# Optimization experiments

Measured on AMD Instinct MI355X. Metric: run time of the kernel, lower is better.

Reference implementation:

```python
import jax, jax.numpy as jnp
import numpy as np

B = 1
L_IMG, L_TMP, L_TXT = 1024, 1024, 256
D, H, HD, MLP = 1024, 16, 64, 4096
L = L_TXT + L_IMG + L_TMP
EPS = 1e-6
ATTN_SCALE = float(1.0 / np.sqrt(HD))


def setup_inputs() -> dict:
    key = jax.random.key(0)
    ks = jax.random.split(key, 12)
    s = 0.02  # keep activations stable
    return {
        'img': jax.random.normal(ks[0], (B, L_IMG, D), jnp.float32),
        'temporal': jax.random.normal(ks[1], (B, L_TMP, D), jnp.float32),
        'txt': jax.random.normal(ks[2], (B, L_TXT, D), jnp.float32),
        'vec': jax.random.normal(ks[3], (B, D), jnp.float32),
        'pe': jax.random.normal(ks[4], (B, 1, L, HD // 2, 2, 2), jnp.float32),
        'mod_w': jax.random.normal(ks[5], (3, D, 6 * D), jnp.float32) * s,
        'mod_b': jnp.zeros((3, 6 * D), jnp.float32),
        'qkv_w': jax.random.normal(ks[6], (3, D, 3 * D), jnp.float32) * s,
        'q_scale': jnp.ones((3, HD), jnp.float32),
        'k_scale': jnp.ones((3, HD), jnp.float32),
        'proj_w': jax.random.normal(ks[7], (3, D, D), jnp.float32) * s,
        'proj_b': jnp.zeros((3, D), jnp.float32),
        'mlp_w1': jax.random.normal(ks[8], (3, D, MLP), jnp.float32) * s,
        'mlp_b1': jnp.zeros((3, MLP), jnp.float32),
        'mlp_w2': jax.random.normal(ks[9], (3, MLP, D), jnp.float32) * s,
        'mlp_b2': jnp.zeros((3, D), jnp.float32),
    }


def _ln(x):
    # LayerNorm, elementwise_affine=False, eps=1e-6
    m = jnp.mean(x, axis=-1, keepdims=True)
    v = jnp.mean((x - m) ** 2, axis=-1, keepdims=True)
    return (x - m) * jax.lax.rsqrt(v + EPS)


def _rms(x, scale):
    # flux QKNorm RMSNorm with learnable per-head-dim scale
    return x * jax.lax.rsqrt(jnp.mean(x * x, axis=-1, keepdims=True) + EPS) * scale


def _rope(x, pe):
    # x: (B,H,L,HD), pe: (B,1,L,HD//2,2,2)
    xr = x.reshape(*x.shape[:-1], -1, 1, 2)
    out = pe[..., 0] * xr[..., 0] + pe[..., 1] * xr[..., 1]  # (B,H,L,HD//2,2)
    return out.reshape(x.shape)


def _forward(img, temporal, txt, vec, pe, mod_w, mod_b, qkv_w, q_scale, k_scale,
             proj_w, proj_b, mlp_w1, mlp_b1, mlp_w2, mlp_b2):
    sv = jax.nn.silu(vec)  # (B,D)

    def mods(i):
        m = (sv @ mod_w[i] + mod_b[i])[:, None, :]  # (B,1,6D)
        return jnp.split(m, 6, axis=-1)  # shift1, scale1, gate1, shift2, scale2, gate2

    def qkv_stream(x, i, shift1, scale1):
        xm = (1.0 + scale1) * _ln(x) + shift1
        qkv = (xm @ qkv_w[i]).reshape(x.shape[0], x.shape[1], 3, H, HD)
        q, k, v = jnp.moveaxis(qkv, 2, 0)  # each (B,Ls,H,HD)
        q = jnp.swapaxes(q, 1, 2)
        k = jnp.swapaxes(k, 1, 2)
        v = jnp.swapaxes(v, 1, 2)  # (B,H,Ls,HD)
        return _rms(q, q_scale[i]), _rms(k, k_scale[i]), v

    i_sh1, i_sc1, i_g1, i_sh2, i_sc2, i_g2 = mods(0)
    t_sh1, t_sc1, t_g1, t_sh2, t_sc2, t_g2 = mods(1)
    x_sh1, x_sc1, x_g1, x_sh2, x_sc2, x_g2 = mods(2)

    img_q, img_k, img_v = qkv_stream(img, 0, i_sh1, i_sc1)
    tmp_q, tmp_k, tmp_v = qkv_stream(temporal, 1, t_sh1, t_sc1)
    txt_q, txt_k, txt_v = qkv_stream(txt, 2, x_sh1, x_sc1)

    q = jnp.concatenate((txt_q, img_q, tmp_q), axis=2)
    k = jnp.concatenate((txt_k, img_k, tmp_k), axis=2)
    # NOTE: faithful to source bug: v concat uses temporal_q, not temporal_v
    v = jnp.concatenate((txt_v, img_v, tmp_q), axis=2)

    q = _rope(q, pe)
    k = _rope(k, pe)
    scores = jnp.einsum('bhqd,bhkd->bhqk', q, k) * ATTN_SCALE
    attn = jnp.einsum('bhqk,bhkd->bhqd', jax.nn.softmax(scores, axis=-1), v)
    attn = jnp.swapaxes(attn, 1, 2).reshape(attn.shape[0], L, H * HD)  # (B,L,D)

    txt_a = attn[:, :L_TXT]
    img_a = attn[:, L_TXT:L_TXT + L_IMG]
    tmp_a = attn[:, L_TXT + L_IMG:]

    def mlp(x, i):
        return jax.nn.gelu(x @ mlp_w1[i] + mlp_b1[i], approximate=True) @ mlp_w2[i] + mlp_b2[i]

    img = img + i_g1 * (img_a @ proj_w[0] + proj_b[0])
    img = img + i_g2 * mlp((1.0 + i_sc2) * _ln(img) + i_sh2, 0)
    temporal = temporal + t_g1 * (tmp_a @ proj_w[1] + proj_b[1])
    # NOTE: faithful to source bug: temporal_norm2 is applied to (updated) img
    temporal = temporal + t_g2 * mlp((1.0 + t_sc2) * _ln(img) + t_sh2, 1)
    txt = txt + x_g1 * (txt_a @ proj_w[2] + proj_b[2])
    txt = txt + x_g2 * mlp((1.0 + x_sc2) * _ln(txt) + x_sh2, 2)
    return img, temporal, txt


def reference(img, temporal, txt, vec, pe, mod_w, mod_b, qkv_w, q_scale, k_scale,
              proj_w, proj_b, mlp_w1, mlp_b1, mlp_w2, mlp_b2):
    return _forward(img, temporal, txt, vec, pe, mod_w, mod_b, qkv_w, q_scale,
                    k_scale, proj_w, proj_b, mlp_w1, mlp_b1, mlp_w2, mlp_b2)
```

## Files before the change

### kernel.cpp

```cpp
#include <hip/hip_runtime.h>
#include <hip/hip_bf16.h>

#define L_TXT 256
#define L_IMG 1024
#define L_TMP 1024
#define LTOT  2304
#define DMODEL 1024
#define NH 16
#define HDIM 64
#define DMLP 4096
#define EPSV 1e-6f

typedef unsigned short ushort;
typedef __attribute__((ext_vector_type(8))) short short8b;
typedef __attribute__((ext_vector_type(8))) unsigned short ushort8v;
typedef __attribute__((ext_vector_type(4))) float f32x4;
typedef __attribute__((ext_vector_type(4))) unsigned short ushort4v;

#define MOD_OFF    ((size_t)0)
#define XM_OFF     ((size_t)73728)
#define QKV_OFF    ((size_t)4792320)
#define QB_OFF     ((size_t)18948096)
#define KB_OFF     ((size_t)23666688)
#define VTB_OFF    ((size_t)28385280)
#define ATT_OFF    ((size_t)33103872)
#define S1_OFF     ((size_t)37822464)
#define QKVWT_OFF  ((size_t)49356800)
#define PROJWT_OFF ((size_t)68231168)
#define W1T_OFF    ((size_t)74522624)
#define W2T_OFF    ((size_t)99688448)
#define W2T_END    ((size_t)124854272)

static __device__ __forceinline__ ushort f2bf(float x) {
    __hip_bfloat16 b = __float2bfloat16(x);
    return *reinterpret_cast<ushort*>(&b);
}
static __device__ __forceinline__ float bf2f(ushort u) {
    return __uint_as_float(((unsigned)u) << 16);
}

typedef __attribute__((address_space(1))) const unsigned char gas_t;
typedef __attribute__((address_space(3))) unsigned char las_t;
static __device__ __forceinline__ void gload16(const void* g, void* l) {
    __builtin_amdgcn_global_load_lds((gas_t*)g, (las_t*)l, 16, 0, 0);
}

__global__ __launch_bounds__(256) void k_conv(const float* __restrict__ vec,
                                              const float* __restrict__ modw,
                                              const float* __restrict__ modb,
                                              float* __restrict__ mod,
                                              const float* __restrict__ qkvw,
                                              const float* __restrict__ projw,
                                              const float* __restrict__ w1,
                                              const float* __restrict__ w2,
                                              ushort* __restrict__ qkvwt,
                                              ushort* __restrict__ projwt,
                                              ushort* __restrict__ w1t,
                                              ushort* __restrict__ w2t) {
    __shared__ float tb[64][65];
    int bid = blockIdx.x;
    int tid = threadIdx.x;
    if (bid < 144) {
        __shared__ float svs[DMODEL];
        __shared__ float pl[8][128];
        float4 vv = *reinterpret_cast<const float4*>(vec + tid*4);
        float4 sv4;
        sv4.x = vv.x / (1.0f + __expf(-vv.x));
        sv4.y = vv.y / (1.0f + __expf(-vv.y));
        sv4.z = vv.z / (1.0f + __expf(-vv.z));
        sv4.w = vv.w / (1.0f + __expf(-vv.w));
        *reinterpret_cast<float4*>(&svs[tid*4]) = sv4;
        __syncthreads();
        int g0 = bid * 128;
        int i  = g0 / 6144;
        int j0 = g0 - i * 6144;
        int jl = tid & 31, ko = tid >> 5;
        const float* wp = modw + (size_t)i * 1024 * 6144 + j0 + jl*4;
        float4 acc = {0.f,0.f,0.f,0.f};
        for (int kk = 0; kk < 128; kk++) {
            int k = kk*8 + ko;
            float4 wv = *reinterpret_cast<const float4*>(wp + (size_t)k * 6144);
            float s = svs[k];
            acc.x += s*wv.x; acc.y += s*wv.y; acc.z += s*wv.z; acc.w += s*wv.w;
        }
        pl[ko][jl*4+0] = acc.x; pl[ko][jl*4+1] = acc.y;
        pl[ko][jl*4+2] = acc.z; pl[ko][jl*4+3] = acc.w;
        __syncthreads();
        if (tid < 128) {
            float s = 0.f;
#pragma unroll
            for (int k = 0; k < 8; k++) s += pl[k][tid];
            mod[g0 + tid] = s + modb[g0 + tid];
        }
        return;
    }
    int b = bid - 144;
    const float* W; ushort* WT; int K, N, nt, kt;
    if (b < 2304) {
        int s = b / 768, r = b % 768;
        K = 1024; N = 3072; nt = r % 48; kt = r / 48;
        W = qkvw + (size_t)s * K * N; WT = qkvwt + (size_t)s * N * K;
    } else if (b < 3072) {
        b -= 2304; int s = b / 256, r = b % 256;
        K = 1024; N = 1024; nt = r % 16; kt = r / 16;
        W = projw + (size_t)s * K * N; WT = projwt + (size_t)s * N * K;
    } else if (b < 6144) {
        b -= 3072; int s = b / 1024, r = b % 1024;
        K = 1024; N = 4096; nt = r % 64; kt = r / 64;
        W = w1 + (size_t)s * K * N; WT = w1t + (size_t)s * N * K;
    } else {
        b -= 6144; int s = b / 1024, r = b % 1024;
        K = 4096; N = 1024; nt = r % 16; kt = r / 16;
        W = w2 + (size_t)s * K * N; WT = w2t + (size_t)s * N * K;
    }
    {
        int r = tid >> 4, c4 = (tid & 15) * 4;
#pragma unroll
        for (int i = 0; i < 4; i++) {
            float4 v = *reinterpret_cast<const float4*>(W + (size_t)(kt*64 + r + i*16) * N + nt*64 + c4);
            tb[r + i*16][c4+0] = v.x; tb[r + i*16][c4+1] = v.y;
            tb[r + i*16][c4+2] = v.z; tb[r + i*16][c4+3] = v.w;
        }
    }
    __syncthreads();
    {
        int n = tid >> 2, ks = (tid & 3) * 16;
        ushort8v u0, u1;
#pragma unroll
        for (int i = 0; i < 8; i++) u0[i] = f2bf(tb[ks+i][n]);
#pragma unroll
        for (int i = 0; i < 8; i++) u1[i] = f2bf(tb[ks+8+i][n]);
        ushort* dst = WT + (size_t)(nt*64 + n) * K + kt*64 + ks;
        *reinterpret_cast<ushort8v*>(dst)     = u0;
        *reinterpret_cast<ushort8v*>(dst + 8) = u1;
    }
}

__global__ __launch_bounds__(256) void k_conv_slice(const float* __restrict__ W,
                                                    ushort* __restrict__ WT,
                                                    int K, int N) {
    __shared__ float tb[64][65];
    int nt = blockIdx.x, kt = blockIdx.y, tid = threadIdx.x;
    {
        int r = tid >> 4, c4 = (tid & 15) * 4;
#pragma unroll
        for (int i = 0; i < 4; i++) {
            float4 v = *reinterpret_cast<const float4*>(W + (size_t)(kt*64 + r + i*16) * N + nt*64 + c4);
            tb[r + i*16][c4+0] = v.x; tb[r + i*16][c4+1] = v.y;
            tb[r + i*16][c4+2] = v.z; tb[r + i*16][c4+3] = v.w;
        }
    }
    __syncthreads();
    {
        int n = tid >> 2, ks = (tid & 3) * 16;
        ushort8v u0, u1;
#pragma unroll
        for (int i = 0; i < 8; i++) u0[i] = f2bf(tb[ks+i][n]);
#pragma unroll
        for (int i = 0; i < 8; i++) u1[i] = f2bf(tb[ks+8+i][n]);
        ushort* dst = WT + (size_t)(nt*64 + n) * K + kt*64 + ks;
        *reinterpret_cast<ushort8v*>(dst)     = u0;
        *reinterpret_cast<ushort8v*>(dst + 8) = u1;
    }
}

__global__ __launch_bounds__(256) void k_ln_mod1(const float* __restrict__ img,
                                                 const float* __restrict__ tmp,
                                                 const float* __restrict__ txt,
                                                 const float* __restrict__ mod,
                                                 ushort* __restrict__ xm) {
    int l = blockIdx.x;
    const float* src; int strm;
    if (l < L_TXT)              { src = txt + (size_t)l * DMODEL;            strm = 2; }
    else if (l < L_TXT + L_IMG) { src = img + (size_t)(l - L_TXT) * DMODEL;  strm = 0; }
    else                        { src = tmp + (size_t)(l - L_TXT - L_IMG) * DMODEL; strm = 1; }

    int d = threadIdx.x * 4;
    float4 x = *reinterpret_cast<const float4*>(src + d);
    float s  = x.x + x.y + x.z + x.w;
    float s2 = x.x*x.x + x.y*x.y + x.z*x.z + x.w*x.w;
#pragma unroll
    for (int o = 32; o > 0; o >>= 1) { s += __shfl_xor(s, o); s2 += __shfl_xor(s2, o); }
    __shared__ float red[8];
    int wave = threadIdx.x >> 6, lane = threadIdx.x & 63;
    if (lane == 0) { red[wave*2] = s; red[wave*2+1] = s2; }
    __syncthreads();
    if (threadIdx.x == 0) {
        float a = 0.f, b = 0.f;
        for (int w = 0; w < 4; w++) { a += red[w*2]; b += red[w*2+1]; }
        red[0] = a; red[1] = b;
    }
    __syncthreads();
    float mean = red[0] * (1.0f/DMODEL);
    float var  = red[1] * (1.0f/DMODEL) - mean*mean;
    float inv  = rsqrtf(var + EPSV);

    const float* sh = mod + strm*6144;
    const float* sc = sh + 1024;
    float4 shv = *reinterpret_cast<const float4*>(sh + d);
    float4 scv = *reinterpret_cast<const float4*>(sc + d);
    ushort4v o;
    o.x = f2bf((1.f+scv.x)*((x.x-mean)*inv) + shv.x);
    o.y = f2bf((1.f+scv.y)*((x.y-mean)*inv) + shv.y);
    o.z = f2bf((1.f+scv.z)*((x.z-mean)*inv) + shv.z);
    o.w = f2bf((1.f+scv.w)*((x.w-mean)*inv) + shv.w);
    *reinterpret_cast<ushort4v*>(xm + (size_t)l*DMODEL + d) = o;
}

__global__ __launch_bounds__(256) void k_ln_mod2(const float* __restrict__ src,
                                                 const float* __restrict__ sh,
                                                 const float* __restrict__ sc,
                                                 ushort* __restrict__ out) {
    int r = blockIdx.x;
    const float* srow = src + (size_t)r * DMODEL;
    int d = threadIdx.x * 4;
    float4 x = *reinterpret_cast<const float4*>(srow + d);
    float s  = x.x + x.y + x.z + x.w;
    float s2 = x.x*x.x + x.y*x.y + x.z*x.z + x.w*x.w;
#pragma unroll
    for (int o = 32; o > 0; o >>= 1) { s += __shfl_xor(s, o); s2 += __shfl_xor(s2, o); }
    __shared__ float red[8];
    int wave = threadIdx.x >> 6, lane = threadIdx.x & 63;
    if (lane == 0) { red[wave*2] = s; red[wave*2+1] = s2; }
    __syncthreads();
    if (threadIdx.x == 0) {
        float a = 0.f, b = 0.f;
        for (int w = 0; w < 4; w++) { a += red[w*2]; b += red[w*2+1]; }
        red[0] = a; red[1] = b;
    }
    __syncthreads();
    float mean = red[0] * (1.0f/DMODEL);
    float var  = red[1] * (1.0f/DMODEL) - mean*mean;
    float inv  = rsqrtf(var + EPSV);
    float4 shv = *reinterpret_cast<const float4*>(sh + d);
    float4 scv = *reinterpret_cast<const float4*>(sc + d);
    ushort4v o;
    o.x = f2bf((1.f+scv.x)*((x.x-mean)*inv) + shv.x);
    o.y = f2bf((1.f+scv.y)*((x.y-mean)*inv) + shv.y);
    o.z = f2bf((1.f+scv.z)*((x.z-mean)*inv) + shv.z);
    o.w = f2bf((1.f+scv.w)*((x.w-mean)*inv) + shv.w);
    *reinterpret_cast<ushort4v*>(out + (size_t)r*DMODEL + d) = o;
}

__global__ __launch_bounds__(256) void k_ln_modg(const float* __restrict__ s1,
                                                 const float* __restrict__ mod,
                                                 ushort* __restrict__ xm) {
    int row = blockIdx.x;
    int strm = row < 256 ? 2 : 0;
    const float* srow = s1 + (size_t)row * DMODEL;
    int d = threadIdx.x * 4;
    float4 x = *reinterpret_cast<const float4*>(srow + d);
    float s  = x.x + x.y + x.z + x.w;
    float s2 = x.x*x.x + x.y*x.y + x.z*x.z + x.w*x.w;
#pragma unroll
    for (int o = 32; o > 0; o >>= 1) { s += __shfl_xor(s, o); s2 += __shfl_xor(s2, o); }
    __shared__ float red[8];
    int wave = threadIdx.x >> 6, lane = threadIdx.x & 63;
    if (lane == 0) { red[wave*2] = s; red[wave*2+1] = s2; }
    __syncthreads();
    if (threadIdx.x == 0) {
        float a = 0.f, b = 0.f;
        for (int w = 0; w < 4; w++) { a += red[w*2]; b += red[w*2+1]; }
        red[0] = a; red[1] = b;
    }
    __syncthreads();
    float mean = red[0] * (1.0f/DMODEL);
    float var  = red[1] * (1.0f/DMODEL) - mean*mean;
    float inv  = rsqrtf(var + EPSV);
    const float* sh = mod + strm*6144 + 3*1024;
    const float* sc = mod + strm*6144 + 4*1024;
    float4 shv = *reinterpret_cast<const float4*>(sh + d);
    float4 scv = *reinterpret_cast<const float4*>(sc + d);
    ushort4v o;
    o.x = f2bf((1.f+scv.x)*((x.x-mean)*inv) + shv.x);
    o.y = f2bf((1.f+scv.y)*((x.y-mean)*inv) + shv.y);
    o.z = f2bf((1.f+scv.z)*((x.z-mean)*inv) + shv.z);
    o.w = f2bf((1.f+scv.w)*((x.w-mean)*inv) + shv.w);
    *reinterpret_cast<ushort4v*>(xm + (size_t)row*DMODEL + d) = o;
}

__device__ __forceinline__ float gelu_fast(float x) {
    return x / (1.0f + __expf(-1.5957691216057308f * (x + 0.044715f * x * x * x)));
}

template<int MODE, int BM, typename OutT>
__global__ __launch_bounds__(256) void k_gemm_ms(const ushort* __restrict__ A_t,
                                                 const ushort* __restrict__ A_i,
                                                 const ushort* __restrict__ A_m,
                                                 const ushort* __restrict__ BT,
                                                 const float* __restrict__ bias,
                                                 const float* __restrict__ res_t,
                                                 const float* __restrict__ res_i,
                                                 const float* __restrict__ res_m,
                                                 const float* __restrict__ mod, int gidx,
                                                 OutT* __restrict__ out_t,
                                                 OutT* __restrict__ out_i,
                                                 OutT* __restrict__ out_m,
                                                 int N, int K, int ry0) {
    constexpr int MI = BM / 32;
    const int brow = (ry0 + blockIdx.y) * BM;
    int s, lrow;
    if (brow < 256)       { s = 2; lrow = brow; }
    else if (brow < 1280) { s = 0; lrow = brow - 256; }
    else                  { s = 1; lrow = brow - 1280; }

    const ushort* A = (s==2 ? A_t : s==0 ? A_i : A_m) + (size_t)lrow * K;
    const ushort* BTs = BT + (size_t)s * N * K;
    const float* bi = bias ? bias + (size_t)s * N : nullptr;
    const float* resl = (MODE==2) ? ((s==2 ? res_t : s==0 ? res_i : res_m) + (size_t)lrow * N) : nullptr;
    const float* gate = (MODE==2) ? (mod + s*6144 + gidx*1024) : nullptr;
    OutT* Cl = (s==2 ? out_t : s==0 ? out_i : out_m) + (size_t)lrow * N;

    __shared__ ushort Asl[BM*64];
    __shared__ ushort Bsl[128*64];
    const int tid = threadIdx.x;
    const int lane = tid & 63, w = tid >> 6;
    const int wr = w >> 1, wc = w & 1;
    const int bn = blockIdx.x * 128;
    const int r15 = lane & 15, g4 = lane >> 4;

    f32x4 acc[MI][4];
#pragma unroll
    for (int i = 0; i < MI; i++)
#pragma unroll
        for (int j = 0; j < 4; j++) acc[i][j] = (f32x4){0.f,0.f,0.f,0.f};

    for (int k0 = 0; k0 < K; k0 += 64) {
#pragma unroll
        for (int i = 0; i < BM/32; i++) {
            int chunk = i*4 + w;
            int seg = chunk*64 + lane;
            int row = seg >> 3;
            int gs  = (seg & 7) ^ (row & 7);
            gload16(A + (size_t)row * K + k0 + gs*8, Asl + (size_t)chunk * 512);
        }
#pragma unroll
        for (int i = 0; i < 4; i++) {
            int chunk = i*4 + w;
            int seg = chunk*64 + lane;
            int row = seg >> 3;
            int gs  = (seg & 7) ^ (row & 7);
            gload16(BTs + (size_t)(bn + row) * K + k0 + gs*8, Bsl + (size_t)chunk * 512);
        }
        __syncthreads();
#pragma unroll
        for (int kk = 0; kk < 2; kk++) {
            short8b a[MI], b[4];
#pragma unroll
            for (int mi = 0; mi < MI; mi++) {
                int row = wr*(MI*16) + mi*16 + r15;
                int c   = kk*4 + g4;
                a[mi] = *reinterpret_cast<const short8b*>(&Asl[row*64 + ((c ^ (row & 7)))*8]);
            }
#pragma unroll
            for (int ni = 0; ni < 4; ni++) {
                int row = wc*64 + ni*16 + r15;
                int c   = kk*4 + g4;
                b[ni] = *reinterpret_cast<const short8b*>(&Bsl[row*64 + ((c ^ (row & 7)))*8]);
            }
#pragma unroll
            for (int mi = 0; mi < MI; mi++)
#pragma unroll
                for (int ni = 0; ni < 4; ni++)
                    acc[mi][ni] = __builtin_amdgcn_mfma_f32_16x16x32_bf16(a[mi], b[ni], acc[mi][ni], 0, 0, 0);
        }
        __syncthreads();
    }

#pragma unroll
    for (int mi = 0; mi < MI; mi++) {
#pragma unroll
        for (int ni = 0; ni < 4; ni++) {
            int col = bn + wc*64 + ni*16 + r15;
            float bv = bi ? bi[col] : 0.f;
#pragma unroll
            for (int r = 0; r < 4; r++) {
                int rr = wr*(MI*16) + mi*16 + g4*4 + r;
                float v = acc[mi][ni][r] + bv;
                if (MODE == 1) v = gelu_fast(v);
                if (MODE == 2) v = resl[(size_t)rr * N + col] + gate[col] * v;
                if (sizeof(OutT) == 2) Cl[(size_t)rr * N + col] = (OutT)f2bf(v);
                else                   Cl[(size_t)rr * N + col] = (OutT)v;
            }
        }
    }
}

__global__ __launch_bounds__(256) void k_qkvfin(const ushort* __restrict__ qkv,
                                                const float* __restrict__ pe,
                                                const float* __restrict__ qs,
                                                const float* __restrict__ ks,
                                                ushort* __restrict__ Q,
                                                ushort* __restrict__ K,
                                                ushort* __restrict__ VT) {
    const int tid = threadIdx.x;
    const int w = tid >> 6, lane = tid & 63;
    const int h  = blockIdx.x / 36;
    const int l0 = (blockIdx.x % 36) * 64;
    __shared__ ushort vbuf[64][65];

    for (int it = 0; it < 16; it++) {
        int ll = it*4 + w;
        int l = l0 + ll;
        int strm;
        if (l < L_TXT) strm = 2; else if (l < L_TXT + L_IMG) strm = 0; else strm = 1;
        const ushort* row = qkv + (size_t)l * 3 * DMODEL + h*HDIM + lane;
        float q = bf2f(row[0]);
        float k = bf2f(row[DMODEL]);
        float v = bf2f(row[2*DMODEL]);

        float sq = q*q, sk = k*k;
#pragma unroll
        for (int o = 32; o > 0; o >>= 1) { sq += __shfl_xor(sq, o); sk += __shfl_xor(sk, o); }
        float rq = q * rsqrtf(sq * (1.0f/HDIM) + EPSV) * qs[strm*HDIM + lane];
        float rk = k * rsqrtf(sk * (1.0f/HDIM) + EPSV) * ks[strm*HDIM + lane];

        float vout = (strm == 1) ? rq : v;

        float rq_p = __shfl_xor(rq, 1);
        float rk_p = __shfl_xor(rk, 1);
        float qe = (lane & 1) ? rq_p : rq;
        float qo = (lane & 1) ? rq : rq_p;
        float ke = (lane & 1) ? rk_p : rk;
        float ko = (lane & 1) ? rk : rk_p;
        const float* pel = pe + (size_t)l*128 + (lane >> 1)*4 + (lane & 1)*2;
        float qr = pel[0]*qe + pel[1]*qo;
        float kr = pel[0]*ke + pel[1]*ko;

        size_t idx = ((size_t)h * LTOT + l) * HDIM + lane;
        Q[idx] = f2bf(qr);
        K[idx] = f2bf(kr);
        vbuf[ll][lane] = f2bf(vout);
    }
    __syncthreads();
    {
        int d = tid >> 2, ls = (tid & 3) * 16;
        ushort8v u0, u1;
#pragma unroll
        for (int i = 0; i < 8; i++) u0[i] = vbuf[ls+i][d];
#pragma unroll
        for (int i = 0; i < 8; i++) u1[i] = vbuf[ls+8+i][d];
        ushort* dst = VT + ((size_t)h * 64 + d) * LTOT + l0 + ls;
        *reinterpret_cast<ushort8v*>(dst)     = u0;
        *reinterpret_cast<ushort8v*>(dst + 8) = u1;
    }
}

__global__ __launch_bounds__(256) void k_attn_mfma(const ushort* __restrict__ Qb,
                                                   const ushort* __restrict__ Kb,
                                                   const ushort* __restrict__ VTb,
                                                   ushort* __restrict__ att) {
    const int tid = threadIdx.x;
    const int w = tid >> 6, lane = tid & 63;
    const int h  = blockIdx.x / 36;
    const int qt = blockIdx.x % 36;
    const int qbase = qt*64 + w*16;
    const int g = lane >> 4;
    const int q = lane & 15;

    __shared__ ushort Ksl[2][64*64];
    __shared__ ushort Vsl[2][64*64];
    __shared__ ushort plds[4][1024];
    ushort* P = plds[w];

    const ushort* Kg = Kb  + (size_t)h * LTOT * 64;
    const ushort* Vg = VTb + (size_t)h * 64 * LTOT;

    const ushort* qp = Qb + ((size_t)h * LTOT + qbase + q) * 64 + g*8;
    const short8b qf0 = *reinterpret_cast<const short8b*>(qp);
    const short8b qf1 = *reinterpret_cast<const short8b*>(qp + 32);

    f32x4 out[4];
#pragma unroll
    for (int d = 0; d < 4; d++) out[d] = (f32x4){0.f,0.f,0.f,0.f};
    float m = -1e30f, lsum = 0.f;

#pragma unroll
    for (int i = 0; i < 2; i++) {
        int seg = i*256 + tid;
        int row = seg >> 3;
        int gs  = (seg & 7) ^ (row & 7);
        gload16(Kg + (size_t)row*64 + gs*8, &Ksl[0][(size_t)(i*256 + w*64)*8]);
        gload16(Vg + (size_t)row*LTOT + gs*8, &Vsl[0][(size_t)(i*256 + w*64)*8]);
    }

    for (int t = 0; t < 36; t++) {
        const int cb = t & 1;
        __syncthreads();
        if (t < 35) {
            int kvn = (t+1) * 64;
#pragma unroll
            for (int i = 0; i < 2; i++) {
                int seg = i*256 + tid;
                int row = seg >> 3;
                int gs  = (seg & 7) ^ (row & 7);
                gload16(Kg + (size_t)(kvn + row)*64 + gs*8, &Ksl[cb^1][(size_t)(i*256 + w*64)*8]);
                gload16(Vg + (size_t)row*LTOT + kvn + gs*8, &Vsl[cb^1][(size_t)(i*256 + w*64)*8]);
            }
        }

        f32x4 s[4];
        __builtin_amdgcn_s_setprio(1);
#pragma unroll
        for (int ks = 0; ks < 4; ks++) {
            int r = ks*16 + q;
            short8b kf0 = *reinterpret_cast<const short8b*>(&Ksl[cb][r*64 + ((g     ^ (r & 7)))*8]);
            short8b kf1 = *reinterpret_cast<const short8b*>(&Ksl[cb][r*64 + (((4+g) ^ (r & 7)))*8]);
            f32x4 acc = (f32x4){0.f,0.f,0.f,0.f};
            acc = __builtin_amdgcn_mfma_f32_16x16x32_bf16(kf0, qf0, acc, 0, 0, 0);
            acc = __builtin_amdgcn_mfma_f32_16x16x32_bf16(kf1, qf1, acc, 0, 0, 0);
            s[ks] = acc;
        }
        __builtin_amdgcn_s_setprio(0);
        float tmax = -1e30f;
#pragma unroll
        for (int ks = 0; ks < 4; ks++)
#pragma unroll
            for (int r = 0; r < 4; r++) tmax = fmaxf(tmax, s[ks][r]);
        tmax = fmaxf(tmax, __shfl_xor(tmax, 16));
        tmax = fmaxf(tmax, __shfl_xor(tmax, 32));
        float newm = fmaxf(m, tmax * 0.125f);
        float c = __expf(m - newm);
        float p[16];
        float tsum = 0.f;
#pragma unroll
        for (int ks = 0; ks < 4; ks++)
#pragma unroll
            for (int r = 0; r < 4; r++) {
                float pv = __expf(s[ks][r] * 0.125f - newm);
                p[ks*4+r] = pv;
                tsum += pv;
            }
        tsum += __shfl_xor(tsum, 16);
        tsum += __shfl_xor(tsum, 32);
        lsum = lsum * c + tsum;
        m = newm;
#pragma unroll
        for (int d = 0; d < 4; d++) out[d] *= c;

#pragma unroll
        for (int ks = 0; ks < 4; ks++) {
            ushort4v pk;
            pk.x = f2bf(p[ks*4+0]); pk.y = f2bf(p[ks*4+1]);
            pk.z = f2bf(p[ks*4+2]); pk.w = f2bf(p[ks*4+3]);
            int widx = (q*64 + ks*16 + g*4) ^ ((q & 7) << 3);
            *reinterpret_cast<ushort4v*>(&P[widx]) = pk;
        }
        __builtin_amdgcn_s_setprio(1);
#pragma unroll
        for (int c2 = 0; c2 < 2; c2++) {
            int ridx = (q*64 + c2*32 + g*8) ^ ((q & 7) << 3);
            short8b pf = *reinterpret_cast<const short8b*>(&P[ridx]);
#pragma unroll
            for (int ds = 0; ds < 4; ds++) {
                int d = ds*16 + q;
                short8b vf = *reinterpret_cast<const short8b*>(&Vsl[cb][d*64 + (((c2*4+g) ^ (d & 7)))*8]);
                out[ds] = __builtin_amdgcn_mfma_f32_16x16x32_bf16(vf, pf, out[ds], 0, 0, 0);
            }
        }
        __builtin_amdgcn_s_setprio(0);
    }

    float inv = 1.0f / lsum;
    ushort* orow = att + (size_t)(qbase + q) * DMODEL + h * HDIM;
#pragma unroll
    for (int ds = 0; ds < 4; ds++) {
        ushort4v o4;
        o4.x = f2bf(out[ds][0]*inv); o4.y = f2bf(out[ds][1]*inv);
        o4.z = f2bf(out[ds][2]*inv); o4.w = f2bf(out[ds][3]*inv);
        *reinterpret_cast<ushort4v*>(orow + ds*16 + g*4) = o4;
    }
}

extern "C" void kernel_launch(void* const* d_in, const int* in_sizes, int n_in,
                              void* d_out, int out_size, void* d_ws, size_t ws_size,
                              hipStream_t stream) {
    const float* img  = (const float*)d_in[0];
    const float* tmp  = (const float*)d_in[1];
    const float* txt  = (const float*)d_in[2];
    const float* vec  = (const float*)d_in[3];
    const float* pe   = (const float*)d_in[4];
    const float* modw = (const float*)d_in[5];
    const float* modb = (const float*)d_in[6];
    const float* qkvw = (const float*)d_in[7];
    const float* qsc  = (const float*)d_in[8];
    const float* ksc  = (const float*)d_in[9];
    const float* projw= (const float*)d_in[10];
    const float* projb= (const float*)d_in[11];
    const float* w1   = (const float*)d_in[12];
    const float* b1   = (const float*)d_in[13];
    const float* w2   = (const float*)d_in[14];
    const float* b2   = (const float*)d_in[15];

    char* wsb = (char*)d_ws;
    float*  mod    = (float*) (wsb + MOD_OFF);
    ushort* xm     = (ushort*)(wsb + XM_OFF);
    ushort* qkv    = (ushort*)(wsb + QKV_OFF);
    ushort* t1     = (ushort*)(wsb + QKV_OFF);
    ushort* Qb     = (ushort*)(wsb + QB_OFF);
    ushort* Kb     = (ushort*)(wsb + KB_OFF);
    ushort* VTb    = (ushort*)(wsb + VTB_OFF);
    ushort* att    = (ushort*)(wsb + ATT_OFF);
    float*  s1     = (float*) (wsb + S1_OFF);
    ushort* qkvwt  = (ushort*)(wsb + QKVWT_OFF);
    ushort* projwt = (ushort*)(wsb + PROJWT_OFF);
    ushort* w1t    = (ushort*)(wsb + W1T_OFF);

    const bool bigws = ws_size >= W2T_END;
    ushort* w2t = bigws ? (ushort*)(wsb + W2T_OFF) : w1t;

    float* out_img = (float*)d_out;
    float* out_tmp = out_img + (size_t)L_IMG * DMODEL;
    float* out_txt = out_tmp + (size_t)L_TMP * DMODEL;

    int conv_blocks = bigws ? (144 + 9216) : (144 + 6144);
    k_conv<<<conv_blocks, 256, 0, stream>>>(vec, modw, modb, mod,
                                            qkvw, projw, w1, w2,
                                            qkvwt, projwt, w1t, w2t);
    k_ln_mod1<<<LTOT, 256, 0, stream>>>(img, tmp, txt, mod, xm);

    k_gemm_ms<0, 128, ushort><<<dim3(24, 18), 256, 0, stream>>>(
        xm, xm + (size_t)256*DMODEL, xm + (size_t)1280*DMODEL,
        qkvwt, nullptr, nullptr, nullptr, nullptr, nullptr, 0,
        qkv, qkv + (size_t)256*3072, qkv + (size_t)1280*3072, 3072, DMODEL, 0);

    k_qkvfin<<<NH*36, 256, 0, stream>>>(qkv, pe, qsc, ksc, Qb, Kb, VTb);
    k_attn_mfma<<<NH*36, 256, 0, stream>>>(Qb, Kb, VTb, att);

    k_gemm_ms<2, 64, float><<<dim3(8, 36), 256, 0, stream>>>(
        att, att + (size_t)256*DMODEL, att + (size_t)1280*DMODEL,
        projwt, projb, txt, img, tmp, mod, 2,
        s1, s1 + (size_t)256*DMODEL, s1 + (size_t)1280*DMODEL, DMODEL, DMODEL, 0);

    k_ln_modg<<<1280, 256, 0, stream>>>(s1, mod, xm);
    k_gemm_ms<1, 128, ushort><<<dim3(32, 10), 256, 0, stream>>>(
        xm, xm + (size_t)256*DMODEL, xm + (size_t)1280*DMODEL,
        w1t, b1, nullptr, nullptr, nullptr, nullptr, 0,
        t1, t1 + (size_t)256*DMLP, t1, DMLP, DMODEL, 0);
    if (!bigws) {
        k_conv_slice<<<dim3(16, 64), 256, 0, stream>>>(w2,                          w1t,                          DMLP, DMODEL);
        k_conv_slice<<<dim3(16, 64), 256, 0, stream>>>(w2 + (size_t)2*DMLP*DMODEL,  w1t + (size_t)2*DMLP*DMODEL,  DMLP, DMODEL);
    }
    k_gemm_ms<2, 64, float><<<dim3(8, 20), 256, 0, stream>>>(
        t1, t1 + (size_t)256*DMLP, t1,
        w2t, b2, s1, s1 + (size_t)256*DMODEL, s1 + (size_t)1280*DMODEL, mod, 5,
        out_txt, out_img, out_tmp, DMODEL, DMLP, 0);

    k_ln_mod2<<<L_TMP, 256, 0, stream>>>(out_img, mod + 1*6144 + 3*1024, mod + 1*6144 + 4*1024, xm + (size_t)1280*DMODEL);
    k_gemm_ms<1, 128, ushort><<<dim3(32, 8), 256, 0, stream>>>(
        xm, xm + (size_t)256*DMODEL, xm + (size_t)1280*DMODEL,
        w1t, b1, nullptr, nullptr, nullptr, nullptr, 0,
        t1, t1, t1, DMLP, DMODEL, 10);
    if (!bigws) {
        k_conv_slice<<<dim3(16, 64), 256, 0, stream>>>(w2 + (size_t)DMLP*DMODEL, w1t + (size_t)DMLP*DMODEL, DMLP, DMODEL);
    }
    k_gemm_ms<2, 64, float><<<dim3(8, 16), 256, 0, stream>>>(
        t1, t1, t1,
        w2t, b2, s1, s1, s1 + (size_t)1280*DMODEL, mod, 5,
        out_txt, out_img, out_tmp, DMODEL, DMLP, 20);
}
```

Before: 354.8 us.

## Split-K the modulation GEMV, retile W2 GEMMs to BN=64, coalesce transpose stores

The modulation matvec is split four ways along K across 576 blocks that write partial sums, and a new small kernel reduces them and adds the bias. This gives that part of the conversion kernel more parallelism at the cost of one extra launch. The GEMM template gains a BN parameter, and the two MLP down-projection launches use 64-wide N tiles so they run twice as many blocks, which helps fill the CUs on these small-N GEMMs. The weight transpose write-back is reorganized so each thread stores one 16-byte chunk for two rows, aiming at more contiguous global writes.

```diff
diff --git a/kernel.cpp b/kernel.cpp
--- a/kernel.cpp
+++ b/kernel.cpp
@@ -47,8 +47,7 @@
 
 __global__ __launch_bounds__(256) void k_conv(const float* __restrict__ vec,
                                               const float* __restrict__ modw,
-                                              const float* __restrict__ modb,
-                                              float* __restrict__ mod,
+                                              float* __restrict__ modp,
                                               const float* __restrict__ qkvw,
                                               const float* __restrict__ projw,
                                               const float* __restrict__ w1,
@@ -60,41 +59,40 @@
     __shared__ float tb[64][65];
     int bid = blockIdx.x;
     int tid = threadIdx.x;
-    if (bid < 144) {
-        __shared__ float svs[DMODEL];
-        __shared__ float pl[8][128];
-        float4 vv = *reinterpret_cast<const float4*>(vec + tid*4);
-        float4 sv4;
-        sv4.x = vv.x / (1.0f + __expf(-vv.x));
-        sv4.y = vv.y / (1.0f + __expf(-vv.y));
-        sv4.z = vv.z / (1.0f + __expf(-vv.z));
-        sv4.w = vv.w / (1.0f + __expf(-vv.w));
-        *reinterpret_cast<float4*>(&svs[tid*4]) = sv4;
-        __syncthreads();
-        int g0 = bid * 128;
+    if (bid < 576) {
+        float* svs = &tb[0][0];
+        float* pl  = &tb[0][0] + 1024;
+        int g0 = (bid >> 2) * 128;
+        int ks = bid & 3;
         int i  = g0 / 6144;
         int j0 = g0 - i * 6144;
+        {
+            float v = vec[ks*256 + tid];
+            svs[tid] = v / (1.0f + __expf(-v));
+        }
+        __syncthreads();
         int jl = tid & 31, ko = tid >> 5;
-        const float* wp = modw + (size_t)i * 1024 * 6144 + j0 + jl*4;
+        const float* wp = modw + (size_t)i * 1024 * 6144 + (size_t)(ks*256) * 6144 + j0 + jl*4;
         float4 acc = {0.f,0.f,0.f,0.f};
-        for (int kk = 0; kk < 128; kk++) {
+#pragma unroll 8
+        for (int kk = 0; kk < 32; kk++) {
             int k = kk*8 + ko;
             float4 wv = *reinterpret_cast<const float4*>(wp + (size_t)k * 6144);
             float s = svs[k];
             acc.x += s*wv.x; acc.y += s*wv.y; acc.z += s*wv.z; acc.w += s*wv.w;
         }
-        pl[ko][jl*4+0] = acc.x; pl[ko][jl*4+1] = acc.y;
-        pl[ko][jl*4+2] = acc.z; pl[ko][jl*4+3] = acc.w;
+        pl[ko*128 + jl*4+0] = acc.x; pl[ko*128 + jl*4+1] = acc.y;
+        pl[ko*128 + jl*4+2] = acc.z; pl[ko*128 + jl*4+3] = acc.w;
         __syncthreads();
         if (tid < 128) {
             float s = 0.f;
 #pragma unroll
-            for (int k = 0; k < 8; k++) s += pl[k][tid];
-            mod[g0 + tid] = s + modb[g0 + tid];
+            for (int k = 0; k < 8; k++) s += pl[k*128 + tid];
+            modp[(size_t)ks*18432 + g0 + tid] = s;
         }
         return;
     }
-    int b = bid - 144;
+    int b = bid - 576;
     const float* W; ushort* WT; int K, N, nt, kt;
     if (b < 2304) {
         int s = b / 768, r = b % 768;
@@ -124,16 +122,25 @@
     }
     __syncthreads();
     {
-        int n = tid >> 2, ks = (tid & 3) * 16;
-        ushort8v u0, u1;
-#pragma unroll
-        for (int i = 0; i < 8; i++) u0[i] = f2bf(tb[ks+i][n]);
-#pragma unroll
-        for (int i = 0; i < 8; i++) u1[i] = f2bf(tb[ks+8+i][n]);
-        ushort* dst = WT + (size_t)(nt*64 + n) * K + kt*64 + ks;
-        *reinterpret_cast<ushort8v*>(dst)     = u0;
-        *reinterpret_cast<ushort8v*>(dst + 8) = u1;
-    }
+        int n  = tid >> 3;
+        int k8 = (tid & 7) * 8;
+#pragma unroll
+        for (int half = 0; half < 2; half++) {
+            int nn = n + half*32;
+            ushort8v u;
+#pragma unroll
+            for (int i = 0; i < 8; i++) u[i] = f2bf(tb[k8+i][nn]);
+            *reinterpret_cast<ushort8v*>(WT + (size_t)(nt*64 + nn) * K + kt*64 + k8) = u;
+        }
+    }
+}
+
+__global__ __launch_bounds__(256) void k_modr(const float* __restrict__ p,
+                                              const float* __restrict__ modb,
+                                              float* __restrict__ mod) {
+    int g = blockIdx.x * 256 + threadIdx.x;
+    float s = p[g] + p[18432 + g] + p[2*18432 + g] + p[3*18432 + g];
+    mod[g] = s + modb[g];
 }
 
 __global__ __launch_bounds__(256) void k_conv_slice(const float* __restrict__ W,
@@ -152,15 +159,16 @@
     }
     __syncthreads();
     {
-        int n = tid >> 2, ks = (tid & 3) * 16;
-        ushort8v u0, u1;
-#pragma unroll
-        for (int i = 0; i < 8; i++) u0[i] = f2bf(tb[ks+i][n]);
-#pragma unroll
-        for (int i = 0; i < 8; i++) u1[i] = f2bf(tb[ks+8+i][n]);
-        ushort* dst = WT + (size_t)(nt*64 + n) * K + kt*64 + ks;
-        *reinterpret_cast<ushort8v*>(dst)     = u0;
-        *reinterpret_cast<ushort8v*>(dst + 8) = u1;
+        int n  = tid >> 3;
+        int k8 = (tid & 7) * 8;
+#pragma unroll
+        for (int half = 0; half < 2; half++) {
+            int nn = n + half*32;
+            ushort8v u;
+#pragma unroll
+            for (int i = 0; i < 8; i++) u[i] = f2bf(tb[k8+i][nn]);
+            *reinterpret_cast<ushort8v*>(WT + (size_t)(nt*64 + nn) * K + kt*64 + k8) = u;
+        }
     }
 }
 
@@ -283,7 +291,7 @@
     return x / (1.0f + __expf(-1.5957691216057308f * (x + 0.044715f * x * x * x)));
 }
 
-template<int MODE, int BM, typename OutT>
+template<int MODE, int BM, int BN, typename OutT>
 __global__ __launch_bounds__(256) void k_gemm_ms(const ushort* __restrict__ A_t,
                                                  const ushort* __restrict__ A_i,
                                                  const ushort* __restrict__ A_m,
@@ -298,6 +306,7 @@
                                                  OutT* __restrict__ out_m,
                                                  int N, int K, int ry0) {
     constexpr int MI = BM / 32;
+    constexpr int NI = BN / 32;
     const int brow = (ry0 + blockIdx.y) * BM;
     int s, lrow;
     if (brow < 256)       { s = 2; lrow = brow; }
@@ -312,18 +321,18 @@
     OutT* Cl = (s==2 ? out_t : s==0 ? out_i : out_m) + (size_t)lrow * N;
 
     __shared__ ushort Asl[BM*64];
-    __shared__ ushort Bsl[128*64];
+    __shared__ ushort Bsl[BN*64];
     const int tid = threadIdx.x;
     const int lane = tid & 63, w = tid >> 6;
     const int wr = w >> 1, wc = w & 1;
-    const int bn = blockIdx.x * 128;
+    const int bn = blockIdx.x * BN;
     const int r15 = lane & 15, g4 = lane >> 4;
 
-    f32x4 acc[MI][4];
+    f32x4 acc[MI][NI];
 #pragma unroll
     for (int i = 0; i < MI; i++)
 #pragma unroll
-        for (int j = 0; j < 4; j++) acc[i][j] = (f32x4){0.f,0.f,0.f,0.f};
+        for (int j = 0; j < NI; j++) acc[i][j] = (f32x4){0.f,0.f,0.f,0.f};
 
     for (int k0 = 0; k0 < K; k0 += 64) {
 #pragma unroll
@@ -335,7 +344,7 @@
             gload16(A + (size_t)row * K + k0 + gs*8, Asl + (size_t)chunk * 512);
         }
 #pragma unroll
-        for (int i = 0; i < 4; i++) {
+        for (int i = 0; i < BN/32; i++) {
             int chunk = i*4 + w;
             int seg = chunk*64 + lane;
             int row = seg >> 3;
@@ -345,7 +354,7 @@
         __syncthreads();
 #pragma unroll
         for (int kk = 0; kk < 2; kk++) {
-            short8b a[MI], b[4];
+            short8b a[MI], b[NI];
 #pragma unroll
             for (int mi = 0; mi < MI; mi++) {
                 int row = wr*(MI*16) + mi*16 + r15;
@@ -353,15 +362,15 @@
                 a[mi] = *reinterpret_cast<const short8b*>(&Asl[row*64 + ((c ^ (row & 7)))*8]);
             }
 #pragma unroll
-            for (int ni = 0; ni < 4; ni++) {
-                int row = wc*64 + ni*16 + r15;
+            for (int ni = 0; ni < NI; ni++) {
+                int row = wc*(NI*16) + ni*16 + r15;
                 int c   = kk*4 + g4;
                 b[ni] = *reinterpret_cast<const short8b*>(&Bsl[row*64 + ((c ^ (row & 7)))*8]);
             }
 #pragma unroll
             for (int mi = 0; mi < MI; mi++)
 #pragma unroll
-                for (int ni = 0; ni < 4; ni++)
+                for (int ni = 0; ni < NI; ni++)
                     acc[mi][ni] = __builtin_amdgcn_mfma_f32_16x16x32_bf16(a[mi], b[ni], acc[mi][ni], 0, 0, 0);
         }
         __syncthreads();
@@ -370,8 +379,8 @@
 #pragma unroll
     for (int mi = 0; mi < MI; mi++) {
 #pragma unroll
-        for (int ni = 0; ni < 4; ni++) {
-            int col = bn + wc*64 + ni*16 + r15;
+        for (int ni = 0; ni < NI; ni++) {
+            int col = bn + wc*(NI*16) + ni*16 + r15;
             float bv = bi ? bi[col] : 0.f;
 #pragma unroll
             for (int r = 0; r < 4; r++) {
@@ -600,6 +609,7 @@
     ushort* Qb     = (ushort*)(wsb + QB_OFF);
     ushort* Kb     = (ushort*)(wsb + KB_OFF);
     ushort* VTb    = (ushort*)(wsb + VTB_OFF);
+    float*  modp   = (float*) (wsb + ATT_OFF);
     ushort* att    = (ushort*)(wsb + ATT_OFF);
     float*  s1     = (float*) (wsb + S1_OFF);
     ushort* qkvwt  = (ushort*)(wsb + QKVWT_OFF);
@@ -613,13 +623,14 @@
     float* out_tmp = out_img + (size_t)L_IMG * DMODEL;
     float* out_txt = out_tmp + (size_t)L_TMP * DMODEL;
 
-    int conv_blocks = bigws ? (144 + 9216) : (144 + 6144);
-    k_conv<<<conv_blocks, 256, 0, stream>>>(vec, modw, modb, mod,
+    int conv_blocks = 576 + (bigws ? 9216 : 6144);
+    k_conv<<<conv_blocks, 256, 0, stream>>>(vec, modw, modp,
                                             qkvw, projw, w1, w2,
                                             qkvwt, projwt, w1t, w2t);
+    k_modr<<<72, 256, 0, stream>>>(modp, modb, mod);
     k_ln_mod1<<<LTOT, 256, 0, stream>>>(img, tmp, txt, mod, xm);
 
-    k_gemm_ms<0, 128, ushort><<<dim3(24, 18), 256, 0, stream>>>(
+    k_gemm_ms<0, 128, 128, ushort><<<dim3(24, 18), 256, 0, stream>>>(
         xm, xm + (size_t)256*DMODEL, xm + (size_t)1280*DMODEL,
         qkvwt, nullptr, nullptr, nullptr, nullptr, nullptr, 0,
         qkv, qkv + (size_t)256*3072, qkv + (size_t)1280*3072, 3072, DMODEL, 0);
@@ -627,13 +638,13 @@
     k_qkvfin<<<NH*36, 256, 0, stream>>>(qkv, pe, qsc, ksc, Qb, Kb, VTb);
     k_attn_mfma<<<NH*36, 256, 0, stream>>>(Qb, Kb, VTb, att);
 
-    k_gemm_ms<2, 64, float><<<dim3(8, 36), 256, 0, stream>>>(
+    k_gemm_ms<2, 64, 128, float><<<dim3(8, 36), 256, 0, stream>>>(
         att, att + (size_t)256*DMODEL, att + (size_t)1280*DMODEL,
         projwt, projb, txt, img, tmp, mod, 2,
         s1, s1 + (size_t)256*DMODEL, s1 + (size_t)1280*DMODEL, DMODEL, DMODEL, 0);
 
     k_ln_modg<<<1280, 256, 0, stream>>>(s1, mod, xm);
-    k_gemm_ms<1, 128, ushort><<<dim3(32, 10), 256, 0, stream>>>(
+    k_gemm_ms<1, 128, 128, ushort><<<dim3(32, 10), 256, 0, stream>>>(
         xm, xm + (size_t)256*DMODEL, xm + (size_t)1280*DMODEL,
         w1t, b1, nullptr, nullptr, nullptr, nullptr, 0,
         t1, t1 + (size_t)256*DMLP, t1, DMLP, DMODEL, 0);
@@ -641,20 +652,20 @@
         k_conv_slice<<<dim3(16, 64), 256, 0, stream>>>(w2,                          w1t,                          DMLP, DMODEL);
         k_conv_slice<<<dim3(16, 64), 256, 0, stream>>>(w2 + (size_t)2*DMLP*DMODEL,  w1t + (size_t)2*DMLP*DMODEL,  DMLP, DMODEL);
     }
-    k_gemm_ms<2, 64, float><<<dim3(8, 20), 256, 0, stream>>>(
+    k_gemm_ms<2, 64, 64, float><<<dim3(16, 20), 256, 0, stream>>>(
         t1, t1 + (size_t)256*DMLP, t1,
         w2t, b2, s1, s1 + (size_t)256*DMODEL, s1 + (size_t)1280*DMODEL, mod, 5,
         out_txt, out_img, out_tmp, DMODEL, DMLP, 0);
 
     k_ln_mod2<<<L_TMP, 256, 0, stream>>>(out_img, mod + 1*6144 + 3*1024, mod + 1*6144 + 4*1024, xm + (size_t)1280*DMODEL);
-    k_gemm_ms<1, 128, ushort><<<dim3(32, 8), 256, 0, stream>>>(
+    k_gemm_ms<1, 128, 128, ushort><<<dim3(32, 8), 256, 0, stream>>>(
         xm, xm + (size_t)256*DMODEL, xm + (size_t)1280*DMODEL,
         w1t, b1, nullptr, nullptr, nullptr, nullptr, 0,
         t1, t1, t1, DMLP, DMODEL, 10);
     if (!bigws) {
         k_conv_slice<<<dim3(16, 64), 256, 0, stream>>>(w2 + (size_t)DMLP*DMODEL, w1t + (size_t)DMLP*DMODEL, DMLP, DMODEL);
     }
-    k_gemm_ms<2, 64, float><<<dim3(8, 16), 256, 0, stream>>>(
+    k_gemm_ms<2, 64, 64, float><<<dim3(16, 16), 256, 0, stream>>>(
         t1, t1, t1,
         w2t, b2, s1, s1, s1 + (size_t)1280*DMODEL, mod, 5,
         out_txt, out_img, out_tmp, DMODEL, DMLP, 20);
```

After: 327.8 us. 1.08x faster.
